# Optimization experiments

Measured on AMD Instinct MI355X. Metric: run time of the kernel, lower is better.

Reference implementation:

```python
import math
import jax, jax.numpy as jnp
import numpy as np

N_NODES = 100000
N_EDGES = 1600000
N_FEATS = 128
HIDDEN = 64
N_CLASSES = 40
N_LAYERS = 8
ALPHA = 0.1
LAMDA = 0.5


def setup_inputs() -> dict:
    key = jax.random.key(0)
    ks = jax.random.split(key, 6)
    x = jax.random.normal(ks[0], (N_NODES, N_FEATS), dtype=jnp.float32)
    edge_index = jax.random.randint(ks[1], (2, N_EDGES), 0, N_NODES, dtype=jnp.int32)
    W0 = jax.random.normal(ks[2], (N_FEATS, HIDDEN), dtype=jnp.float32) / np.sqrt(N_FEATS)
    b0 = jnp.zeros((HIDDEN,), dtype=jnp.float32)
    Wl = jax.random.normal(ks[3], (N_LAYERS, HIDDEN, HIDDEN), dtype=jnp.float32) / np.sqrt(HIDDEN)
    W_out = jax.random.normal(ks[4], (HIDDEN, N_CLASSES), dtype=jnp.float32) / np.sqrt(HIDDEN)
    b_out = jnp.zeros((N_CLASSES,), dtype=jnp.float32)
    return {"x": x, "edge_index": edge_index, "W0": W0, "b0": b0,
            "Wl": Wl, "W_out": W_out, "b_out": b_out}


def _gcn_norm(edge_index, num_nodes, dtype):
    # PyG gcn_norm: add self-loops (fill 1), sym-normalize D^-1/2 A D^-1/2.
    loops = jnp.arange(num_nodes, dtype=edge_index.dtype)
    row = jnp.concatenate([edge_index[0], loops])  # source
    col = jnp.concatenate([edge_index[1], loops])  # target
    w = jnp.ones(row.shape[0], dtype=dtype)
    deg = jax.ops.segment_sum(w, col, num_segments=num_nodes)
    dinv = jnp.where(deg > 0, jax.lax.rsqrt(deg), 0.0).astype(dtype)
    norm = dinv[row] * w * dinv[col]
    return row, col, norm


def _propagate(x, row, col, norm, num_nodes):
    # SpMM: out[i] = sum_{e: col[e]==i} norm[e] * x[row[e]]
    msgs = x[row] * norm[:, None]  # [E+N, H]
    return jax.ops.segment_sum(msgs, col, num_segments=num_nodes)


def reference(x, edge_index, W0, b0, Wl, W_out, b_out):
    n = x.shape[0]
    row, col, norm = _gcn_norm(edge_index, n, x.dtype)
    # eval mode: dropout is identity; non-arxiv dataset: no batchnorm
    h = jax.nn.relu(x @ W0 + b0)
    h0 = h
    for i in range(N_LAYERS):
        agg = _propagate(h, row, col, norm, n)
        support = (1.0 - ALPHA) * agg + ALPHA * h0
        beta = math.log(LAMDA / (i + 1) + 1.0)
        h = jax.nn.relu(beta * (support @ Wl[i]) + (1.0 - beta) * support)
    return h @ W_out + b_out
```

## Files before the change

### kernel.cpp

```cpp
#include <hip/hip_runtime.h>
#include <cmath>

#define N_NODES   100000
#define N_EDGES   1600000
#define N_FEATS   128
#define HIDDEN    64
#define N_CLASSES 40
#define N_LAYERS  8
#define ALPHA     0.1f
#define LAMDA     0.5f

#define SCAN_ITEMS 8
#define SCAN_BLK   256
#define SCAN_TILE  (SCAN_ITEMS * SCAN_BLK)
#define SCAN_NBLK  ((N_NODES + SCAN_TILE - 1) / SCAN_TILE)

typedef unsigned short ushortT;
typedef unsigned int   uintT;

__device__ __forceinline__ float bf2f(ushortT u) {
    return __uint_as_float(((uintT)u) << 16);
}
__device__ __forceinline__ ushortT f2bf(float f) {
    uintT x = __float_as_uint(f);
    return (ushortT)((x + 0x7FFFu + ((x >> 16) & 1u)) >> 16);
}


__global__ __launch_bounds__(256) void k_zero_deg(int* __restrict__ deg) {
    int i = blockIdx.x * 256 + threadIdx.x;
    if (i < N_NODES) deg[i] = 0;
}

__global__ __launch_bounds__(256) void k_count_deg(const int* __restrict__ col,
                                                   int* __restrict__ deg) {
    const int G = gridDim.x * 256;
    int e0 = blockIdx.x * 256 + threadIdx.x;
    int e1 = e0 + G, e2 = e1 + G, e3 = e2 + G;
    int c0 = (e0 < N_EDGES) ? col[e0] : -1;
    int c1 = (e1 < N_EDGES) ? col[e1] : -1;
    int c2 = (e2 < N_EDGES) ? col[e2] : -1;
    int c3 = (e3 < N_EDGES) ? col[e3] : -1;
    if (c0 >= 0) atomicAdd(&deg[c0], 1);
    if (c1 >= 0) atomicAdd(&deg[c1], 1);
    if (c2 >= 0) atomicAdd(&deg[c2], 1);
    if (c3 >= 0) atomicAdd(&deg[c3], 1);
}

__global__ __launch_bounds__(SCAN_BLK) void k_scan1(const int* __restrict__ deg,
                                                    int* __restrict__ rowptr,
                                                    int* __restrict__ bsum) {
    __shared__ int sc[SCAN_BLK];
    const int t = threadIdx.x;
    const int base = blockIdx.x * SCAN_TILE + t * SCAN_ITEMS;
    int v[SCAN_ITEMS];
    int tsum = 0;
#pragma unroll
    for (int j = 0; j < SCAN_ITEMS; ++j) {
        v[j] = (base + j < N_NODES) ? deg[base + j] : 0;
        tsum += v[j];
    }
    sc[t] = tsum;
    __syncthreads();
    for (int off = 1; off < SCAN_BLK; off <<= 1) {
        int x = (t >= off) ? sc[t - off] : 0;
        __syncthreads();
        sc[t] += x;
        __syncthreads();
    }
    int run = sc[t] - tsum;
#pragma unroll
    for (int j = 0; j < SCAN_ITEMS; ++j) {
        if (base + j < N_NODES) rowptr[base + j] = run;
        run += v[j];
    }
    if (t == SCAN_BLK - 1) bsum[blockIdx.x] = sc[SCAN_BLK - 1];
}

__global__ __launch_bounds__(SCAN_BLK) void k_scan2(int* __restrict__ bsum) {
    __shared__ int sc[SCAN_BLK];
    const int t = threadIdx.x;
    int v = (t < SCAN_NBLK) ? bsum[t] : 0;
    sc[t] = v;
    __syncthreads();
    for (int off = 1; off < SCAN_BLK; off <<= 1) {
        int x = (t >= off) ? sc[t - off] : 0;
        __syncthreads();
        sc[t] += x;
        __syncthreads();
    }
    if (t < SCAN_NBLK) bsum[t] = sc[t] - v;
}

__global__ __launch_bounds__(256) void k_scan3(int* __restrict__ rowptr,
                                               const int* __restrict__ bsum,
                                               int* __restrict__ cursor) {
    int i = blockIdx.x * 256 + threadIdx.x;
    if (i < N_NODES) {
        int r = rowptr[i] + bsum[i / SCAN_TILE];
        rowptr[i] = r;
        cursor[i] = r;
    }
    if (i == 0) rowptr[N_NODES] = N_EDGES;
}

__global__ __launch_bounds__(256) void k_dinv(const int* __restrict__ deg,
                                              float* __restrict__ dinv) {
    int i = blockIdx.x * 256 + threadIdx.x;
    if (i < N_NODES) dinv[i] = rsqrtf(1.0f + (float)deg[i]);
}

__global__ __launch_bounds__(256) void k_fill(const int* __restrict__ row,
                                              const int* __restrict__ col,
                                              const float* __restrict__ dinv,
                                              int* __restrict__ cursor,
                                              int2* __restrict__ csr) {
    const int G = gridDim.x * 256;
    int e0 = blockIdx.x * 256 + threadIdx.x;
    int e1 = e0 + G, e2 = e1 + G, e3 = e2 + G;

    int r0 = 0, r1 = 0, r2 = 0, r3 = 0, c0 = -1, c1 = -1, c2 = -1, c3 = -1;
    if (e0 < N_EDGES) { r0 = row[e0]; c0 = col[e0]; }
    if (e1 < N_EDGES) { r1 = row[e1]; c1 = col[e1]; }
    if (e2 < N_EDGES) { r2 = row[e2]; c2 = col[e2]; }
    if (e3 < N_EDGES) { r3 = row[e3]; c3 = col[e3]; }

    int p0 = 0, p1 = 0, p2 = 0, p3 = 0;
    if (c0 >= 0) p0 = atomicAdd(&cursor[c0], 1);
    if (c1 >= 0) p1 = atomicAdd(&cursor[c1], 1);
    if (c2 >= 0) p2 = atomicAdd(&cursor[c2], 1);
    if (c3 >= 0) p3 = atomicAdd(&cursor[c3], 1);

    if (c0 >= 0) csr[p0] = make_int2(r0, __float_as_int((1.0f - ALPHA) * dinv[r0] * dinv[c0]));
    if (c1 >= 0) csr[p1] = make_int2(r1, __float_as_int((1.0f - ALPHA) * dinv[r1] * dinv[c1]));
    if (c2 >= 0) csr[p2] = make_int2(r2, __float_as_int((1.0f - ALPHA) * dinv[r2] * dinv[c2]));
    if (c3 >= 0) csr[p3] = make_int2(r3, __float_as_int((1.0f - ALPHA) * dinv[r3] * dinv[c3]));
}


__global__ __launch_bounds__(256) void k_gemm_in(const float* __restrict__ x,
                                                 const float* __restrict__ W0,
                                                 const float* __restrict__ b0,
                                                 ushortT* __restrict__ h_bf,
                                                 float* __restrict__ h0) {
    __shared__ float sW[N_FEATS * HIDDEN];
    __shared__ float sX[64 * N_FEATS];
    const int v0 = blockIdx.x * 64;
    const bool full = (v0 + 64 <= N_NODES);

    const float4* W4 = (const float4*)W0;
    for (int idx = threadIdx.x; idx < (N_FEATS * HIDDEN) / 4; idx += 256)
        ((float4*)sW)[idx] = W4[idx];
    if (full) {
        const float4* X4 = (const float4*)(x + (size_t)v0 * N_FEATS);
        for (int idx = threadIdx.x; idx < (64 * N_FEATS) / 4; idx += 256)
            ((float4*)sX)[idx] = X4[idx];
    } else {
        for (int idx = threadIdx.x; idx < 64 * N_FEATS; idx += 256) {
            int r = idx >> 7, k = idx & 127;
            int v = v0 + r;
            sX[idx] = (v < N_NODES) ? x[(size_t)v * N_FEATS + k] : 0.0f;
        }
    }
    __syncthreads();

    const int c  = threadIdx.x & 63;
    const int r0 = threadIdx.x >> 6;
    float acc[16];
#pragma unroll
    for (int j = 0; j < 16; ++j) acc[j] = 0.0f;

    for (int k = 0; k < N_FEATS; ++k) {
        float w = sW[k * HIDDEN + c];
#pragma unroll
        for (int j = 0; j < 16; ++j)
            acc[j] += sX[(r0 + 4 * j) * N_FEATS + k] * w;
    }

    const float bias = b0[c];
#pragma unroll
    for (int j = 0; j < 16; ++j) {
        int v = v0 + r0 + 4 * j;
        if (v < N_NODES) {
            float val = fmaxf(acc[j] + bias, 0.0f);
            h_bf[(size_t)v * HIDDEN + c] = f2bf(val);
            h0[(size_t)v * HIDDEN + c]   = val;
        }
    }
}


__global__ __launch_bounds__(256) void k_spmm(const int* __restrict__ rowptr,
                                              const int2* __restrict__ csr,
                                              const float* __restrict__ dinv,
                                              const ushortT* __restrict__ h_bf,
                                              const float* __restrict__ h0,
                                              float* __restrict__ buf) {
    const int lane = threadIdx.x & 63;
    const int l32  = lane & 31;
    const int half = lane >> 5;
    const int node = (blockIdx.x * 256 + threadIdx.x) >> 6;
    if (node >= N_NODES) return;

    const int e0 = rowptr[node];
    const int e1 = rowptr[node + 1];
    const float d = dinv[node];

    float ax, ay;
    if (half == 0) {
        const ushort2 hv = *(const ushort2*)(h_bf + (size_t)node * HIDDEN + 2 * l32);
        const float2 h0v = *(const float2*)(h0 + (size_t)node * HIDDEN + 2 * l32);
        const float cs = (1.0f - ALPHA) * d * d;
        ax = cs * bf2f(hv.x) + ALPHA * h0v.x;
        ay = cs * bf2f(hv.y) + ALPHA * h0v.y;
    } else {
        ax = 0.0f; ay = 0.0f;
    }

    for (int eb = e0; eb < e1; eb += 64) {
        int n = e1 - eb;
        if (n > 64) n = 64;
        int   idx = 0;
        float w   = 0.0f;
        if (lane < n) {
            int2 e = csr[eb + lane];
            idx = e.x;
            w   = __int_as_float(e.y);
        }
        for (int j = 0; j < n; j += 16) {
            int    s[8];
            float  ww[8];
            ushort2 xv[8];
#pragma unroll
            for (int u = 0; u < 8; ++u) {
                int src = j + 2 * u + half;
                s[u]  = __shfl(idx, src);
                ww[u] = __shfl(w, src);
            }
#pragma unroll
            for (int u = 0; u < 8; ++u)
                xv[u] = *(const ushort2*)(h_bf + (size_t)s[u] * HIDDEN + 2 * l32);
#pragma unroll
            for (int u = 0; u < 8; ++u) {
                ax += ww[u] * bf2f(xv[u].x);
                ay += ww[u] * bf2f(xv[u].y);
            }
        }
    }

    ax += __shfl_xor(ax, 32);
    ay += __shfl_xor(ay, 32);
    if (half == 0) {
        float2 o; o.x = ax; o.y = ay;
        *(float2*)(buf + (size_t)node * HIDDEN + 2 * l32) = o;
    }
}


__global__ __launch_bounds__(256) void k_gemm_layer(const float* __restrict__ S,
                                                    const float* __restrict__ W,
                                                    float beta,
                                                    ushortT* __restrict__ hout_bf) {
    __shared__ float sW[HIDDEN * HIDDEN];
    __shared__ float sS[64 * HIDDEN];
    const int v0 = blockIdx.x * 64;
    const bool full = (v0 + 64 <= N_NODES);

    const float4* W4 = (const float4*)W;
    for (int idx = threadIdx.x; idx < (HIDDEN * HIDDEN) / 4; idx += 256)
        ((float4*)sW)[idx] = W4[idx];
    if (full) {
        const float4* S4 = (const float4*)(S + (size_t)v0 * HIDDEN);
        for (int idx = threadIdx.x; idx < (64 * HIDDEN) / 4; idx += 256)
            ((float4*)sS)[idx] = S4[idx];
    } else {
        for (int idx = threadIdx.x; idx < 64 * HIDDEN; idx += 256) {
            int r = idx >> 6, k = idx & 63;
            int v = v0 + r;
            sS[idx] = (v < N_NODES) ? S[(size_t)v * HIDDEN + k] : 0.0f;
        }
    }
    __syncthreads();

    const int c  = threadIdx.x & 63;
    const int r0 = threadIdx.x >> 6;
    float acc[16];
#pragma unroll
    for (int j = 0; j < 16; ++j) acc[j] = 0.0f;

    for (int k = 0; k < HIDDEN; ++k) {
        float w = sW[k * HIDDEN + c];
#pragma unroll
        for (int j = 0; j < 16; ++j)
            acc[j] += sS[(r0 + 4 * j) * HIDDEN + k] * w;
    }

#pragma unroll
    for (int j = 0; j < 16; ++j) {
        int r = r0 + 4 * j;
        int v = v0 + r;
        if (v < N_NODES) {
            float s   = sS[r * HIDDEN + c];
            float val = fmaxf(beta * acc[j] + (1.0f - beta) * s, 0.0f);
            hout_bf[(size_t)v * HIDDEN + c] = f2bf(val);
        }
    }
}


__global__ __launch_bounds__(256) void k_gemm_out(const ushortT* __restrict__ h_bf,
                                                  const float* __restrict__ Wout,
                                                  const float* __restrict__ bout,
                                                  float* __restrict__ out) {
    __shared__ float sW[HIDDEN * N_CLASSES];
    __shared__ float sH[64 * HIDDEN];
    const int v0 = blockIdx.x * 64;
    const bool full = (v0 + 64 <= N_NODES);

    for (int idx = threadIdx.x; idx < HIDDEN * N_CLASSES; idx += 256)
        sW[idx] = Wout[idx];
    if (full) {
        const ushort4* H4 = (const ushort4*)(h_bf + (size_t)v0 * HIDDEN);
        for (int idx = threadIdx.x; idx < (64 * HIDDEN) / 4; idx += 256) {
            ushort4 u = H4[idx];
            sH[idx * 4 + 0] = bf2f(u.x);
            sH[idx * 4 + 1] = bf2f(u.y);
            sH[idx * 4 + 2] = bf2f(u.z);
            sH[idx * 4 + 3] = bf2f(u.w);
        }
    } else {
        for (int idx = threadIdx.x; idx < 64 * HIDDEN; idx += 256) {
            int r = idx >> 6, k = idx & 63;
            int v = v0 + r;
            sH[idx] = (v < N_NODES) ? bf2f(h_bf[(size_t)v * HIDDEN + k]) : 0.0f;
        }
    }
    __syncthreads();

    for (int idx = threadIdx.x; idx < 64 * N_CLASSES; idx += 256) {
        int r = idx / N_CLASSES, c = idx % N_CLASSES;
        int v = v0 + r;
        if (v < N_NODES) {
            float acc = bout[c];
#pragma unroll 8
            for (int k = 0; k < HIDDEN; ++k)
                acc += sH[r * HIDDEN + k] * sW[k * N_CLASSES + c];
            out[(size_t)v * N_CLASSES + c] = acc;
        }
    }
}


extern "C" void kernel_launch(void* const* d_in, const int* in_sizes, int n_in,
                              void* d_out, int out_size, void* d_ws, size_t ws_size,
                              hipStream_t stream) {
    const float* x    = (const float*)d_in[0];
    const int*   ei   = (const int*)d_in[1];
    const float* W0   = (const float*)d_in[2];
    const float* b0   = (const float*)d_in[3];
    const float* Wl   = (const float*)d_in[4];
    const float* Wout = (const float*)d_in[5];
    const float* bout = (const float*)d_in[6];
    float* out = (float*)d_out;

    const int* row = ei;
    const int* col = ei + N_EDGES;

    char* ws = (char*)d_ws;
    size_t off = 0;
    auto alloc = [&](size_t bytes) -> void* {
        void* p = ws + off;
        off += (bytes + 255) & ~(size_t)255;
        return p;
    };
    int*    deg    = (int*)alloc((size_t)N_NODES * 4);
    int*    rowptr = (int*)alloc((size_t)(N_NODES + 1) * 4);
    int*    cursor = (int*)alloc((size_t)N_NODES * 4);
    int*    bsum   = (int*)alloc((size_t)SCAN_NBLK * 4);
    int2*   csr    = (int2*)alloc((size_t)N_EDGES * 8);
    float*  dinv   = (float*)alloc((size_t)N_NODES * 4);
    float*  h0     = (float*)alloc((size_t)N_NODES * HIDDEN * 4);
    float*  buf    = (float*)alloc((size_t)N_NODES * HIDDEN * 4);
    ushortT* h_bf  = (ushortT*)alloc((size_t)N_NODES * HIDDEN * 2);

    const int gN   = (N_NODES + 255) / 256;
    const int gRow = (N_NODES + 63) / 64;
    const int gSpm = (N_NODES * 64 + 255) / 256;
    const int gE4  = (N_EDGES + 4 * 256 - 1) / (4 * 256);

    k_zero_deg <<<gN, 256, 0, stream>>>(deg);
    k_count_deg<<<gE4, 256, 0, stream>>>(col, deg);
    k_scan1    <<<SCAN_NBLK, SCAN_BLK, 0, stream>>>(deg, rowptr, bsum);
    k_scan2    <<<1, SCAN_BLK, 0, stream>>>(bsum);
    k_scan3    <<<gN, 256, 0, stream>>>(rowptr, bsum, cursor);
    k_dinv     <<<gN, 256, 0, stream>>>(deg, dinv);
    k_fill     <<<gE4, 256, 0, stream>>>(row, col, dinv, cursor, csr);

    k_gemm_in<<<gRow, 256, 0, stream>>>(x, W0, b0, h_bf, h0);

    for (int i = 0; i < N_LAYERS; ++i) {
        float beta = logf(LAMDA / (float)(i + 1) + 1.0f);
        k_spmm<<<gSpm, 256, 0, stream>>>(rowptr, csr, dinv, h_bf, h0, buf);
        k_gemm_layer<<<gRow, 256, 0, stream>>>(buf, Wl + (size_t)i * HIDDEN * HIDDEN,
                                               beta, h_bf);
    }

    k_gemm_out<<<gRow, 256, 0, stream>>>(h_bf, Wout, bout, out);
}
```

Measured before the change: 810.5 us.

## Store h0 and SpMM output in bf16, range-partition CSR fill by destination

The initial features h0 and the per-layer aggregated support buffer are now kept in bf16 instead of fp32. This halves the bytes read and written between the SpMM and the layer GEMM, and for the h0 read in every layer. Separately, the CSR fill kernel is restructured so each block handles only edges whose destination falls in one of 8 node ranges, which localizes the cursor atomics and CSR writes. The cost is that every block re-reads the whole col array, plus extra rounding error from bf16 storage of h0 and the aggregates.

```diff
diff --git a/kernel.cpp b/kernel.cpp
--- a/kernel.cpp
+++ b/kernel.cpp
@@ -14,6 +14,10 @@
 #define SCAN_BLK   256
 #define SCAN_TILE  (SCAN_ITEMS * SCAN_BLK)
 #define SCAN_NBLK  ((N_NODES + SCAN_TILE - 1) / SCAN_TILE)
+
+#define FILL_RANGES 8
+#define RANGE_SIZE  ((N_NODES + FILL_RANGES - 1) / FILL_RANGES)
+#define FILL_BLOCKS 1024
 
 typedef unsigned short ushortT;
 typedef unsigned int   uintT;
@@ -115,26 +119,18 @@
                                               const float* __restrict__ dinv,
                                               int* __restrict__ cursor,
                                               int2* __restrict__ csr) {
-    const int G = gridDim.x * 256;
-    int e0 = blockIdx.x * 256 + threadIdx.x;
-    int e1 = e0 + G, e2 = e1 + G, e3 = e2 + G;
-
-    int r0 = 0, r1 = 0, r2 = 0, r3 = 0, c0 = -1, c1 = -1, c2 = -1, c3 = -1;
-    if (e0 < N_EDGES) { r0 = row[e0]; c0 = col[e0]; }
-    if (e1 < N_EDGES) { r1 = row[e1]; c1 = col[e1]; }
-    if (e2 < N_EDGES) { r2 = row[e2]; c2 = col[e2]; }
-    if (e3 < N_EDGES) { r3 = row[e3]; c3 = col[e3]; }
-
-    int p0 = 0, p1 = 0, p2 = 0, p3 = 0;
-    if (c0 >= 0) p0 = atomicAdd(&cursor[c0], 1);
-    if (c1 >= 0) p1 = atomicAdd(&cursor[c1], 1);
-    if (c2 >= 0) p2 = atomicAdd(&cursor[c2], 1);
-    if (c3 >= 0) p3 = atomicAdd(&cursor[c3], 1);
-
-    if (c0 >= 0) csr[p0] = make_int2(r0, __float_as_int((1.0f - ALPHA) * dinv[r0] * dinv[c0]));
-    if (c1 >= 0) csr[p1] = make_int2(r1, __float_as_int((1.0f - ALPHA) * dinv[r1] * dinv[c1]));
-    if (c2 >= 0) csr[p2] = make_int2(r2, __float_as_int((1.0f - ALPHA) * dinv[r2] * dinv[c2]));
-    if (c3 >= 0) csr[p3] = make_int2(r3, __float_as_int((1.0f - ALPHA) * dinv[r3] * dinv[c3]));
+    const int range = blockIdx.x & (FILL_RANGES - 1);
+    const int lo = range * RANGE_SIZE;
+    const int hi = lo + RANGE_SIZE;
+    const int stride = (gridDim.x >> 3) * 256;
+    for (int e = (blockIdx.x >> 3) * 256 + threadIdx.x; e < N_EDGES; e += stride) {
+        int c = col[e];
+        if (c >= lo && c < hi) {
+            int r = row[e];
+            int pos = atomicAdd(&cursor[c], 1);
+            csr[pos] = make_int2(r, __float_as_int((1.0f - ALPHA) * dinv[r] * dinv[c]));
+        }
+    }
 }
 
 
@@ -142,7 +138,7 @@
                                                  const float* __restrict__ W0,
                                                  const float* __restrict__ b0,
                                                  ushortT* __restrict__ h_bf,
-                                                 float* __restrict__ h0) {
+                                                 ushortT* __restrict__ h0_bf) {
     __shared__ float sW[N_FEATS * HIDDEN];
     __shared__ float sX[64 * N_FEATS];
     const int v0 = blockIdx.x * 64;
@@ -182,9 +178,9 @@
     for (int j = 0; j < 16; ++j) {
         int v = v0 + r0 + 4 * j;
         if (v < N_NODES) {
-            float val = fmaxf(acc[j] + bias, 0.0f);
-            h_bf[(size_t)v * HIDDEN + c] = f2bf(val);
-            h0[(size_t)v * HIDDEN + c]   = val;
+            ushortT val = f2bf(fmaxf(acc[j] + bias, 0.0f));
+            h_bf [(size_t)v * HIDDEN + c] = val;
+            h0_bf[(size_t)v * HIDDEN + c] = val;
         }
     }
 }
@@ -194,8 +190,8 @@
                                               const int2* __restrict__ csr,
                                               const float* __restrict__ dinv,
                                               const ushortT* __restrict__ h_bf,
-                                              const float* __restrict__ h0,
-                                              float* __restrict__ buf) {
+                                              const ushortT* __restrict__ h0_bf,
+                                              ushortT* __restrict__ buf_bf) {
     const int lane = threadIdx.x & 63;
     const int l32  = lane & 31;
     const int half = lane >> 5;
@@ -208,11 +204,11 @@
 
     float ax, ay;
     if (half == 0) {
-        const ushort2 hv = *(const ushort2*)(h_bf + (size_t)node * HIDDEN + 2 * l32);
-        const float2 h0v = *(const float2*)(h0 + (size_t)node * HIDDEN + 2 * l32);
+        const ushort2 hv  = *(const ushort2*)(h_bf  + (size_t)node * HIDDEN + 2 * l32);
+        const ushort2 h0v = *(const ushort2*)(h0_bf + (size_t)node * HIDDEN + 2 * l32);
         const float cs = (1.0f - ALPHA) * d * d;
-        ax = cs * bf2f(hv.x) + ALPHA * h0v.x;
-        ay = cs * bf2f(hv.y) + ALPHA * h0v.y;
+        ax = cs * bf2f(hv.x) + ALPHA * bf2f(h0v.x);
+        ay = cs * bf2f(hv.y) + ALPHA * bf2f(h0v.y);
     } else {
         ax = 0.0f; ay = 0.0f;
     }
@@ -251,13 +247,13 @@
     ax += __shfl_xor(ax, 32);
     ay += __shfl_xor(ay, 32);
     if (half == 0) {
-        float2 o; o.x = ax; o.y = ay;
-        *(float2*)(buf + (size_t)node * HIDDEN + 2 * l32) = o;
-    }
-}
-
-
-__global__ __launch_bounds__(256) void k_gemm_layer(const float* __restrict__ S,
+        ushort2 o; o.x = f2bf(ax); o.y = f2bf(ay);
+        *(ushort2*)(buf_bf + (size_t)node * HIDDEN + 2 * l32) = o;
+    }
+}
+
+
+__global__ __launch_bounds__(256) void k_gemm_layer(const ushortT* __restrict__ S_bf,
                                                     const float* __restrict__ W,
                                                     float beta,
                                                     ushortT* __restrict__ hout_bf) {
@@ -270,14 +266,19 @@
     for (int idx = threadIdx.x; idx < (HIDDEN * HIDDEN) / 4; idx += 256)
         ((float4*)sW)[idx] = W4[idx];
     if (full) {
-        const float4* S4 = (const float4*)(S + (size_t)v0 * HIDDEN);
-        for (int idx = threadIdx.x; idx < (64 * HIDDEN) / 4; idx += 256)
-            ((float4*)sS)[idx] = S4[idx];
+        const ushort4* S4 = (const ushort4*)(S_bf + (size_t)v0 * HIDDEN);
+        for (int idx = threadIdx.x; idx < (64 * HIDDEN) / 4; idx += 256) {
+            ushort4 u = S4[idx];
+            sS[idx * 4 + 0] = bf2f(u.x);
+            sS[idx * 4 + 1] = bf2f(u.y);
+            sS[idx * 4 + 2] = bf2f(u.z);
+            sS[idx * 4 + 3] = bf2f(u.w);
+        }
     } else {
         for (int idx = threadIdx.x; idx < 64 * HIDDEN; idx += 256) {
             int r = idx >> 6, k = idx & 63;
             int v = v0 + r;
-            sS[idx] = (v < N_NODES) ? S[(size_t)v * HIDDEN + k] : 0.0f;
+            sS[idx] = (v < N_NODES) ? bf2f(S_bf[(size_t)v * HIDDEN + k]) : 0.0f;
         }
     }
     __syncthreads();
@@ -373,15 +374,15 @@
         off += (bytes + 255) & ~(size_t)255;
         return p;
     };
-    int*    deg    = (int*)alloc((size_t)N_NODES * 4);
-    int*    rowptr = (int*)alloc((size_t)(N_NODES + 1) * 4);
-    int*    cursor = (int*)alloc((size_t)N_NODES * 4);
-    int*    bsum   = (int*)alloc((size_t)SCAN_NBLK * 4);
-    int2*   csr    = (int2*)alloc((size_t)N_EDGES * 8);
-    float*  dinv   = (float*)alloc((size_t)N_NODES * 4);
-    float*  h0     = (float*)alloc((size_t)N_NODES * HIDDEN * 4);
-    float*  buf    = (float*)alloc((size_t)N_NODES * HIDDEN * 4);
-    ushortT* h_bf  = (ushortT*)alloc((size_t)N_NODES * HIDDEN * 2);
+    int*     deg    = (int*)alloc((size_t)N_NODES * 4);
+    int*     rowptr = (int*)alloc((size_t)(N_NODES + 1) * 4);
+    int*     cursor = (int*)alloc((size_t)N_NODES * 4);
+    int*     bsum   = (int*)alloc((size_t)SCAN_NBLK * 4);
+    int2*    csr    = (int2*)alloc((size_t)N_EDGES * 8);
+    float*   dinv   = (float*)alloc((size_t)N_NODES * 4);
+    ushortT* h0_bf  = (ushortT*)alloc((size_t)N_NODES * HIDDEN * 2);
+    ushortT* buf_bf = (ushortT*)alloc((size_t)N_NODES * HIDDEN * 2);
+    ushortT* h_bf   = (ushortT*)alloc((size_t)N_NODES * HIDDEN * 2);
 
     const int gN   = (N_NODES + 255) / 256;
     const int gRow = (N_NODES + 63) / 64;
@@ -394,14 +395,14 @@
     k_scan2    <<<1, SCAN_BLK, 0, stream>>>(bsum);
     k_scan3    <<<gN, 256, 0, stream>>>(rowptr, bsum, cursor);
     k_dinv     <<<gN, 256, 0, stream>>>(deg, dinv);
-    k_fill     <<<gE4, 256, 0, stream>>>(row, col, dinv, cursor, csr);
-
-    k_gemm_in<<<gRow, 256, 0, stream>>>(x, W0, b0, h_bf, h0);
+    k_fill     <<<FILL_BLOCKS, 256, 0, stream>>>(row, col, dinv, cursor, csr);
+
+    k_gemm_in<<<gRow, 256, 0, stream>>>(x, W0, b0, h_bf, h0_bf);
 
     for (int i = 0; i < N_LAYERS; ++i) {
         float beta = logf(LAMDA / (float)(i + 1) + 1.0f);
-        k_spmm<<<gSpm, 256, 0, stream>>>(rowptr, csr, dinv, h_bf, h0, buf);
-        k_gemm_layer<<<gRow, 256, 0, stream>>>(buf, Wl + (size_t)i * HIDDEN * HIDDEN,
+        k_spmm<<<gSpm, 256, 0, stream>>>(rowptr, csr, dinv, h_bf, h0_bf, buf_bf);
+        k_gemm_layer<<<gRow, 256, 0, stream>>>(buf_bf, Wl + (size_t)i * HIDDEN * HIDDEN,
                                                beta, h_bf);
     }
 
```

Result: no change. 798.0 us (-1.5%).
